# Kernel tuning notes

Hardware: AMD Instinct MI355X
Metric: run time of the kernel (lower is better)

Reference implementation:

```python
import jax, jax.numpy as jnp
import numpy as np

M_GROUPS = 512  # fixed number of segments (== fill_max for ii)


def setup_inputs() -> dict:
    key = jax.random.key(0)
    ks = jax.random.split(key, 8)
    B, N, D = 4, 16384, 384
    x = jax.random.normal(ks[0], (B, N, D), dtype=jnp.float32)
    ii = jax.random.randint(ks[1], (N,), 0, M_GROUPS)
    s = 1.0 / np.sqrt(D)
    f_w = jax.random.uniform(ks[2], (D, D), jnp.float32, -s, s)
    f_b = jax.random.uniform(ks[3], (D,), jnp.float32, -s, s)
    g_w = jax.random.uniform(ks[4], (D, D), jnp.float32, -s, s)
    g_b = jax.random.uniform(ks[5], (D,), jnp.float32, -s, s)
    h_w = jax.random.uniform(ks[6], (D, D), jnp.float32, -s, s)
    h_b = jax.random.uniform(ks[7], (D,), jnp.float32, -s, s)
    return {"x": x, "ii": ii, "f_w": f_w, "f_b": f_b,
            "g_w": g_w, "g_b": g_b, "h_w": h_w, "h_b": h_b}


def reference(x, ii, f_w, f_b, g_w, g_b, h_w, h_b):
    # x: [B, N, D], ii: [N] group indices in [0, M_GROUPS)
    logits = x @ g_w.T + g_b                      # g(x): [B, N, D]
    exp_logits = jnp.exp(logits)
    # segment sum over n for each group m (== one-hot einsum 'bnm,bnd->bmd')
    seg = lambda e: jax.ops.segment_sum(e, ii, num_segments=M_GROUPS)
    sum_exp = jax.vmap(seg)(exp_logits)           # [B, M, D]
    denom = sum_exp[:, ii]                        # gather back: [B, N, D]
    w = exp_logits / (denom + 1e-6)
    fx = x @ f_w.T + f_b                          # f(x): [B, N, D]
    y = jax.vmap(seg)(fx * w)                     # [B, M, D]
    y = y @ h_w.T + h_b                           # h(y)
    return y[:, ii]                               # expand: [B, N, D]
```

## Files before the change

kernel.cpp:

```cpp
#include <hip/hip_runtime.h>
#include <hip/hip_bf16.h>

#define D 384
#define NROWS 16384
#define BATCH 4
#define MG 512
#define RTOT (BATCH * NROWS)
#define NC (2 * D)
#define JB 64
#define NJB (D / JB)
#define BM 128
#define BK 32
#define NKT (D / BK)
#define NMT (RTOT / BM)

typedef __attribute__((ext_vector_type(8))) short bf16x8;
typedef __attribute__((ext_vector_type(4))) float f32x4;

static __device__ __forceinline__ unsigned short f2bf(float f) {
  unsigned int u = __float_as_uint(f);
  unsigned int r = u + 0x7fffu + ((u >> 16) & 1u);
  return (unsigned short)(r >> 16);
}
static __device__ __forceinline__ unsigned int cvtpk(float lo, float hi) {
  unsigned int r;
  asm("v_cvt_pk_bf16_f32 %0, %1, %2" : "=v"(r) : "v"(lo), "v"(hi));
  return r;
}
static __device__ __forceinline__ float frcp(float f) {
  float r;
  asm("v_rcp_f32 %0, %1" : "=v"(r) : "v"(f));
  return r;
}

typedef __attribute__((address_space(1))) const void gvoid_t;
typedef __attribute__((address_space(3))) void lvoid_t;
static __device__ __forceinline__ void gl16(const void* g, void* l) {
  __builtin_amdgcn_global_load_lds((gvoid_t*)g, (lvoid_t*)l, 16, 0, 0);
}

__global__ __launch_bounds__(256) void k_convert(const float* __restrict__ x,
                                                 unsigned short* __restrict__ xb) {
  const long total8 = (long)RTOT * D / 8;
  for (long i = blockIdx.x * (long)blockDim.x + threadIdx.x; i < total8;
       i += (long)gridDim.x * blockDim.x) {
    const float4 v0 = ((const float4*)x)[2 * i];
    const float4 v1 = ((const float4*)x)[2 * i + 1];
    int4 o;
    o.x = cvtpk(v0.x, v0.y);
    o.y = cvtpk(v0.z, v0.w);
    o.z = cvtpk(v1.x, v1.y);
    o.w = cvtpk(v1.z, v1.w);
    ((int4*)xb)[i] = o;
  }
}

__global__ __launch_bounds__(512) void k_prep(
    const int* __restrict__ ii, const float* __restrict__ g_w,
    const float* __restrict__ f_w, const float* __restrict__ h_w,
    unsigned short* __restrict__ wt2, unsigned short* __restrict__ hw,
    int* __restrict__ csr_rows, int* __restrict__ grp_sorted,
    float* __restrict__ s12) {
  __shared__ int cnt[MG];
  __shared__ int scan[MG];
  const int blk = blockIdx.x;
  const int t = threadIdx.x;
  if (blk == 0) {
    cnt[t] = 0;
    __syncthreads();
    for (int n = t; n < NROWS; n += MG) atomicAdd(&cnt[ii[n]], 1);
    __syncthreads();
    const int v = cnt[t];
    scan[t] = v;
    __syncthreads();
#pragma unroll
    for (int o = 1; o < MG; o <<= 1) {
      int u = (t >= o) ? scan[t - o] : 0;
      __syncthreads();
      scan[t] += u;
      __syncthreads();
    }
    cnt[t] = scan[t] - v;
    __syncthreads();
    for (int n = t; n < NROWS; n += MG) {
      int m = ii[n];
      int pos = atomicAdd(&cnt[m], 1);
      csr_rows[pos] = n;
      grp_sorted[pos] = m;
    }
  } else if (blk < 64) {
    const int tot4 = 2 * BATCH * MG * D / 4;
    float4 z = {0.f, 0.f, 0.f, 0.f};
    for (int i = (blk - 1) * 512 + t; i < tot4; i += 63 * 512) ((float4*)s12)[i] = z;
  } else {
    const int tid0 = (blk - 64) * 512 + t;
    const int stride = 64 * 512;
    for (int idx = tid0; idx < NC * D; idx += stride) {
      int jblk = idx / (128 * D);
      int rem = idx % (128 * D);
      int c = rem / D, k = rem % D;
      int j = jblk * JB + (c & 63);
      float v = (c < JB) ? g_w[j * D + k] : f_w[j * D + k];
      wt2[idx] = f2bf(v);
    }
    for (int idx = tid0; idx < D * D; idx += stride) hw[idx] = f2bf(h_w[idx]);
  }
}

__global__ __launch_bounds__(256, 4) void k_gemm1(
    const unsigned short* __restrict__ xb, const unsigned short* __restrict__ wt2,
    const float* __restrict__ g_b, const float* __restrict__ f_b,
    const int* __restrict__ csr_rows, const int* __restrict__ grp_sorted,
    float* __restrict__ s1acc, float* __restrict__ s2acc) {
  __shared__ __attribute__((aligned(16))) unsigned short As[2][BM * BK];
  __shared__ __attribute__((aligned(16))) unsigned short Bs[2][BM * BK];
  __shared__ int grpS[BM];

  const int wg = blockIdx.x;
  const int xcd = wg & 7;
  const int ix = wg >> 3;
  const int mt = xcd * (NMT / 8) + ix / NJB;
  const int jb = ix % NJB;
  const int b = mt >> 7;
  const int ib = (mt & 127) * BM;
  const int j0 = jb * JB;

  const int tid = threadIdx.x;
  const int lane = tid & 63, wid = tid >> 6;
  const int wr = wid >> 1, wc = wid & 1;

  if (tid < BM) grpS[tid] = grp_sorted[ib + tid];

  const int srow = wid * 32 + (lane >> 2);
  const int skb = (((lane & 3) ^ ((lane >> 3) & 3))) * 16;
  const int arow0 = b * NROWS + csr_rows[ib + srow];
  const int arow1 = b * NROWS + csr_rows[ib + srow + 16];
  const char* aS0 = (const char*)xb + (size_t)arow0 * (D * 2) + skb;
  const char* aS1 = (const char*)xb + (size_t)arow1 * (D * 2) + skb;
  const char* bS0 = (const char*)wt2 + (size_t)jb * (128 * D * 2) + (size_t)srow * (D * 2) + skb;
  const char* bS1 = bS0 + 16 * (D * 2);

  f32x4 acc[4][4];
#pragma unroll
  for (int m = 0; m < 4; m++)
#pragma unroll
    for (int n = 0; n < 4; n++) acc[m][n] = (f32x4){0.f, 0.f, 0.f, 0.f};

  {
    char* ad = (char*)As[0] + wid * 2048;
    char* bd = (char*)Bs[0] + wid * 2048;
    gl16(aS0, ad); gl16(aS1, ad + 1024);
    gl16(bS0, bd); gl16(bS1, bd + 1024);
  }
  __syncthreads();

  const int swz16 = (((lane >> 4) ^ ((lane >> 1) & 3))) * 16;

#pragma unroll 1
  for (int kt = 0; kt < NKT; ++kt) {
    const int cur = kt & 1;
    if (kt < NKT - 1) {
      const int kb = (kt + 1) * (BK * 2);
      char* ad = (char*)As[cur ^ 1] + wid * 2048;
      char* bd = (char*)Bs[cur ^ 1] + wid * 2048;
      gl16(aS0 + kb, ad); gl16(aS1 + kb, ad + 1024);
      gl16(bS0 + kb, bd); gl16(bS1 + kb, bd + 1024);
    }
    bf16x8 af[4], bfv[4];
#pragma unroll
    for (int m = 0; m < 4; m++)
      af[m] = *(const bf16x8*)((const char*)&As[cur][0] +
                               (wr * 64 + m * 16 + (lane & 15)) * 64 + swz16);
#pragma unroll
    for (int n = 0; n < 4; n++) {
      const int c = (n < 2) ? (wc * 32 + n * 16) : (64 + wc * 32 + (n - 2) * 16);
      bfv[n] = *(const bf16x8*)((const char*)&Bs[cur][0] + (c + (lane & 15)) * 64 + swz16);
    }
#pragma unroll
    for (int m = 0; m < 4; m++)
#pragma unroll
      for (int n = 0; n < 4; n++)
        acc[m][n] = __builtin_amdgcn_mfma_f32_16x16x32_bf16(af[m], bfv[n], acc[m][n], 0, 0, 0);
    __syncthreads();
  }

  const int jA = j0 + wc * 32 + (lane & 15);
  const float gb0 = g_b[jA], gb1 = g_b[jA + 16];
  const float fb0 = f_b[jA], fb1 = f_b[jA + 16];

  int gmr[4][4];
#pragma unroll
  for (int m = 0; m < 4; m++)
#pragma unroll
    for (int r = 0; r < 4; r++)
      gmr[m][r] = grpS[wr * 64 + m * 16 + (lane >> 4) * 4 + r];

#pragma unroll
  for (int m = 0; m < 4; m++)
#pragma unroll
    for (int r = 0; r < 4; r++) {
      const float e0 = expf(acc[m][0][r] + gb0);
      const float e1 = expf(acc[m][1][r] + gb1);
      const float f0 = acc[m][2][r] + fb0;
      const float f1 = acc[m][3][r] + fb1;
      acc[m][0][r] = e0; acc[m][1][r] = e1;
      acc[m][2][r] = f0 * e0; acc[m][3][r] = f1 * e1;
    }

  const int gLo = grpS[wr * 64], gHi = grpS[wr * 64 + 63];
  for (int g = gLo; g <= gHi; ++g) {
    float v0 = 0.f, v1 = 0.f, v2 = 0.f, v3 = 0.f;
#pragma unroll
    for (int m = 0; m < 4; m++)
#pragma unroll
      for (int r = 0; r < 4; r++)
        if (gmr[m][r] == g) {
          v0 += acc[m][0][r]; v1 += acc[m][1][r];
          v2 += acc[m][2][r]; v3 += acc[m][3][r];
        }
    v0 += __shfl_xor(v0, 16); v0 += __shfl_xor(v0, 32);
    v1 += __shfl_xor(v1, 16); v1 += __shfl_xor(v1, 32);
    v2 += __shfl_xor(v2, 16); v2 += __shfl_xor(v2, 32);
    v3 += __shfl_xor(v3, 16); v3 += __shfl_xor(v3, 32);
    if (lane < 16) {
      float* s1p = s1acc + ((size_t)(b * MG + g)) * D + j0 + wc * 32 + lane;
      float* s2p = s2acc + ((size_t)(b * MG + g)) * D + j0 + wc * 32 + lane;
      atomicAdd(s1p, v0);
      atomicAdd(s1p + 16, v1);
      atomicAdd(s2p, v2);
      atomicAdd(s2p + 16, v3);
    }
  }
}

__global__ __launch_bounds__(256) void k_gemm2(
    const float* __restrict__ s1, const float* __restrict__ s2,
    const unsigned short* __restrict__ hw, const float* __restrict__ h_b,
    float* __restrict__ outpre) {
  const int tid = threadIdx.x, lane = tid & 63, wid = tid >> 6;
  const int r0 = blockIdx.y * 16;
  const int c0 = blockIdx.x * 64 + wid * 16;
  f32x4 acc = (f32x4){0.f, 0.f, 0.f, 0.f};
  const int arow = r0 + (lane & 15);
  const float* s1p = s1 + (size_t)arow * D + (lane >> 4) * 8;
  const float* s2p = s2 + (size_t)arow * D + (lane >> 4) * 8;
  const unsigned short* bRow = hw + (size_t)(c0 + (lane & 15)) * D + (lane >> 4) * 8;
#pragma unroll
  for (int kt = 0; kt < D / 32; kt++) {
    float4 u0 = *(const float4*)(s1p + kt * 32);
    float4 u1 = *(const float4*)(s1p + kt * 32 + 4);
    float4 w0 = *(const float4*)(s2p + kt * 32);
    float4 w1 = *(const float4*)(s2p + kt * 32 + 4);
    int4 yi;
    yi.x = cvtpk(w0.x * frcp(u0.x + 1e-6f), w0.y * frcp(u0.y + 1e-6f));
    yi.y = cvtpk(w0.z * frcp(u0.z + 1e-6f), w0.w * frcp(u0.w + 1e-6f));
    yi.z = cvtpk(w1.x * frcp(u1.x + 1e-6f), w1.y * frcp(u1.y + 1e-6f));
    yi.w = cvtpk(w1.z * frcp(u1.z + 1e-6f), w1.w * frcp(u1.w + 1e-6f));
    bf16x8 af = *(bf16x8*)&yi;
    bf16x8 bf_ = *(const bf16x8*)(bRow + kt * 32);
    acc = __builtin_amdgcn_mfma_f32_16x16x32_bf16(af, bf_, acc, 0, 0, 0);
  }
  const int col = c0 + (lane & 15);
  const float hb = h_b[col];
#pragma unroll
  for (int r = 0; r < 4; r++) {
    const int row = r0 + (lane >> 4) * 4 + r;
    outpre[(size_t)row * D + col] = acc[r] + hb;
  }
}

__global__ void k_gather(const float* __restrict__ outpre, const int* __restrict__ ii,
                         float* __restrict__ out) {
  const long total4 = (long)RTOT * (D / 4);
  for (long i = blockIdx.x * (long)blockDim.x + threadIdx.x; i < total4;
       i += (long)gridDim.x * blockDim.x) {
    const long row = i / (D / 4);
    const int q = (int)(i % (D / 4));
    const int b = (int)(row >> 14);
    const int n = (int)(row & (NROWS - 1));
    const int g = ii[n];
    ((float4*)out)[i] = ((const float4*)outpre)[((size_t)(b * MG + g)) * (D / 4) + q];
  }
}

extern "C" void kernel_launch(void* const* d_in, const int* in_sizes, int n_in,
                              void* d_out, int out_size, void* d_ws, size_t ws_size,
                              hipStream_t stream) {
  const float* x = (const float*)d_in[0];
  const int* ii = (const int*)d_in[1];
  const float* f_w = (const float*)d_in[2];
  const float* f_b = (const float*)d_in[3];
  const float* g_w = (const float*)d_in[4];
  const float* g_b = (const float*)d_in[5];
  const float* h_w = (const float*)d_in[6];
  const float* h_b = (const float*)d_in[7];
  float* out = (float*)d_out;

  char* ws = (char*)d_ws;
  size_t off = 0;
  auto alloc = [&](size_t bytes) {
    size_t p = off;
    off = (off + bytes + 255) & ~(size_t)255;
    return p;
  };
  unsigned short* xb = (unsigned short*)(ws + alloc((size_t)RTOT * D * 2));
  unsigned short* wt2 = (unsigned short*)(ws + alloc((size_t)NC * D * 2));
  unsigned short* hw = (unsigned short*)(ws + alloc((size_t)D * D * 2));
  float* s1acc = (float*)(ws + alloc((size_t)BATCH * MG * D * 4));
  float* s2acc = (float*)(ws + alloc((size_t)BATCH * MG * D * 4));
  float* outpre = (float*)(ws + alloc((size_t)BATCH * MG * D * 4));
  int* csr_rows = (int*)(ws + alloc((size_t)NROWS * 4));
  int* grp_sorted = (int*)(ws + alloc((size_t)NROWS * 4));

  k_prep<<<dim3(128), dim3(512), 0, stream>>>(ii, g_w, f_w, h_w, wt2, hw, csr_rows,
                                              grp_sorted, s1acc);
  k_convert<<<dim3(4096), dim3(256), 0, stream>>>(x, xb);
  k_gemm1<<<dim3(NJB * NMT), dim3(256), 0, stream>>>(xb, wt2, g_b, f_b, csr_rows,
                                                     grp_sorted, s1acc, s2acc);
  k_gemm2<<<dim3(D / 64, (BATCH * MG) / 16), dim3(256), 0, stream>>>(s1acc, s2acc, hw, h_b,
                                                                     outpre);
  k_gather<<<dim3(4096), dim3(256), 0, stream>>>(outpre, ii, out);
}
```

Measured before the change: 155.6 us.

## Make gemm1 persistent with resident weight slice and pre-permuted sorted input rows

```diff
diff --git a/kernel.cpp b/kernel.cpp
--- a/kernel.cpp
+++ b/kernel.cpp
@@ -9,10 +9,7 @@
 #define NC (2 * D)
 #define JB 64
 #define NJB (D / JB)
-#define BM 128
-#define BK 32
-#define NKT (D / BK)
-#define NMT (RTOT / BM)
+#define NKT 12
 
 typedef __attribute__((ext_vector_type(8))) short bf16x8;
 typedef __attribute__((ext_vector_type(4))) float f32x4;
@@ -37,22 +34,6 @@
 typedef __attribute__((address_space(3))) void lvoid_t;
 static __device__ __forceinline__ void gl16(const void* g, void* l) {
   __builtin_amdgcn_global_load_lds((gvoid_t*)g, (lvoid_t*)l, 16, 0, 0);
-}
-
-__global__ __launch_bounds__(256) void k_convert(const float* __restrict__ x,
-                                                 unsigned short* __restrict__ xb) {
-  const long total8 = (long)RTOT * D / 8;
-  for (long i = blockIdx.x * (long)blockDim.x + threadIdx.x; i < total8;
-       i += (long)gridDim.x * blockDim.x) {
-    const float4 v0 = ((const float4*)x)[2 * i];
-    const float4 v1 = ((const float4*)x)[2 * i + 1];
-    int4 o;
-    o.x = cvtpk(v0.x, v0.y);
-    o.y = cvtpk(v0.z, v0.w);
-    o.z = cvtpk(v1.x, v1.y);
-    o.w = cvtpk(v1.z, v1.w);
-    ((int4*)xb)[i] = o;
-  }
 }
 
 __global__ __launch_bounds__(512) void k_prep(
@@ -107,38 +88,61 @@
   }
 }
 
-__global__ __launch_bounds__(256, 4) void k_gemm1(
-    const unsigned short* __restrict__ xb, const unsigned short* __restrict__ wt2,
+__global__ __launch_bounds__(256) void k_convert(const float* __restrict__ x,
+                                                 const int* __restrict__ csr_rows,
+                                                 unsigned short* __restrict__ xp) {
+  const int g = blockIdx.x * 256 + threadIdx.x;
+  const int orow = g / 48;
+  const int c = g - orow * 48;
+  const int bb = orow >> 14;
+  const int ir = csr_rows[orow & (NROWS - 1)];
+  const float* src = x + ((size_t)(bb << 14) + ir) * D + c * 8;
+  const float4 v0 = ((const float4*)src)[0];
+  const float4 v1 = ((const float4*)src)[1];
+  int4 o;
+  o.x = cvtpk(v0.x, v0.y);
+  o.y = cvtpk(v0.z, v0.w);
+  o.z = cvtpk(v1.x, v1.y);
+  o.w = cvtpk(v1.z, v1.w);
+  ((int4*)xp)[g] = o;
+}
+
+__global__ __launch_bounds__(512, 1) void k_gemm1(
+    const unsigned short* __restrict__ xp, const unsigned short* __restrict__ wt2,
     const float* __restrict__ g_b, const float* __restrict__ f_b,
-    const int* __restrict__ csr_rows, const int* __restrict__ grp_sorted,
-    float* __restrict__ s1acc, float* __restrict__ s2acc) {
-  __shared__ __attribute__((aligned(16))) unsigned short As[2][BM * BK];
-  __shared__ __attribute__((aligned(16))) unsigned short Bs[2][BM * BK];
-  __shared__ int grpS[BM];
-
-  const int wg = blockIdx.x;
-  const int xcd = wg & 7;
-  const int ix = wg >> 3;
-  const int mt = xcd * (NMT / 8) + ix / NJB;
-  const int jb = ix % NJB;
-  const int b = mt >> 7;
-  const int ib = (mt & 127) * BM;
-  const int j0 = jb * JB;
+    const int* __restrict__ grp_sorted, float* __restrict__ s1acc,
+    float* __restrict__ s2acc) {
+  __shared__ __attribute__((aligned(16))) unsigned short Bs[12 * 4096];
+  __shared__ __attribute__((aligned(16))) unsigned short As[4 * 8192];
 
   const int tid = threadIdx.x;
   const int lane = tid & 63, wid = tid >> 6;
-  const int wr = wid >> 1, wc = wid & 1;
-
-  if (tid < BM) grpS[tid] = grp_sorted[ib + tid];
-
-  const int srow = wid * 32 + (lane >> 2);
-  const int skb = (((lane & 3) ^ ((lane >> 3) & 3))) * 16;
-  const int arow0 = b * NROWS + csr_rows[ib + srow];
-  const int arow1 = b * NROWS + csr_rows[ib + srow + 16];
-  const char* aS0 = (const char*)xb + (size_t)arow0 * (D * 2) + skb;
-  const char* aS1 = (const char*)xb + (size_t)arow1 * (D * 2) + skb;
-  const char* bS0 = (const char*)wt2 + (size_t)jb * (128 * D * 2) + (size_t)srow * (D * 2) + skb;
-  const char* bS1 = bS0 + 16 * (D * 2);
+  const int h = wid >> 2;
+  const int w4 = wid & 3;
+  const int wr = w4 >> 1, wc = w4 & 1;
+  const int q0 = blockIdx.x * 6;
+  const int pair0 = q0 & 255;
+
+  const int skb = ((lane & 3) ^ ((lane >> 3) & 3)) * 16;
+  const int swz16 = ((lane >> 4) ^ ((lane >> 1) & 3)) * 16;
+
+  const char* p0 = (const char*)xp +
+                   ((size_t)(pair0 * 256 + h * 128 + w4 * 32 + (lane >> 2))) * (D * 2) + skb;
+  const char* p1 = p0 + 16 * (D * 2);
+  int ipair = pair0;
+
+  char* const AsB = (char*)As;
+  char* const BsB = (char*)Bs;
+  const int adoff = h * 8192 + w4 * 2048;
+
+#pragma unroll
+  for (int s = 0; s < 3; ++s) {
+    char* ad = AsB + s * 16384 + adoff;
+    gl16(p0, ad);
+    gl16(p1, ad + 1024);
+    p0 += 64;
+    p1 += 64;
+  }
 
   f32x4 acc[4][4];
 #pragma unroll
@@ -146,90 +150,115 @@
 #pragma unroll
     for (int n = 0; n < 4; n++) acc[m][n] = (f32x4){0.f, 0.f, 0.f, 0.f};
 
-  {
-    char* ad = (char*)As[0] + wid * 2048;
-    char* bd = (char*)Bs[0] + wid * 2048;
-    gl16(aS0, ad); gl16(aS1, ad + 1024);
-    gl16(bS0, bd); gl16(bS1, bd + 1024);
-  }
-  __syncthreads();
-
-  const int swz16 = (((lane >> 4) ^ ((lane >> 1) & 3))) * 16;
-
+  int jbprev = -1;
 #pragma unroll 1
-  for (int kt = 0; kt < NKT; ++kt) {
-    const int cur = kt & 1;
-    if (kt < NKT - 1) {
-      const int kb = (kt + 1) * (BK * 2);
-      char* ad = (char*)As[cur ^ 1] + wid * 2048;
-      char* bd = (char*)Bs[cur ^ 1] + wid * 2048;
-      gl16(aS0 + kb, ad); gl16(aS1 + kb, ad + 1024);
-      gl16(bS0 + kb, bd); gl16(bS1 + kb, bd + 1024);
-    }
-    bf16x8 af[4], bfv[4];
+  for (int e = 0; e < 6; ++e) {
+    const int q = q0 + e;
+    const int jb = q >> 8;
+    const int pair = q & 255;
+    const bool jch = (jb != jbprev);
+    jbprev = jb;
+    const char* wtj = (const char*)wt2 + (size_t)jb * (128 * D * 2);
+
+#pragma unroll
+    for (int kt = 0; kt < NKT; ++kt) {
+      asm volatile("s_waitcnt vmcnt(4)\ns_barrier" ::: "memory");
+      if (kt == 0 && jch) {
+#pragma unroll
+        for (int i = 0; i < 12; ++i)
+          gl16(wtj + (size_t)(tid >> 2) * (D * 2) + i * 64 + skb,
+               BsB + i * 8192 + wid * 1024);
+        asm volatile("s_waitcnt vmcnt(0)\ns_barrier" ::: "memory");
+      }
+      {
+        char* ad = AsB + ((kt + 3) & 3) * 16384 + adoff;
+        gl16(p0, ad);
+        gl16(p1, ad + 1024);
+        if (kt == 8) {
+          p0 += 195904; p1 += 195904;
+          if (++ipair == 256) {
+            ipair = 0;
+            p0 -= (size_t)256 * 196608;
+            p1 -= (size_t)256 * 196608;
+          }
+        } else {
+          p0 += 64; p1 += 64;
+        }
+      }
+      bf16x8 af[4], bfv[4];
+      const char* ab = AsB + (kt & 3) * 16384 + h * 8192;
+#pragma unroll
+      for (int m = 0; m < 4; m++)
+        af[m] = *(const bf16x8*)(ab + (wr * 64 + m * 16 + (lane & 15)) * 64 + swz16);
+      const char* bbp = BsB + kt * 8192;
+#pragma unroll
+      for (int n = 0; n < 4; n++) {
+        const int c = (n < 2) ? (wc * 32 + n * 16) : (64 + wc * 32 + (n - 2) * 16);
+        bfv[n] = *(const bf16x8*)(bbp + (c + (lane & 15)) * 64 + swz16);
+      }
+#pragma unroll
+      for (int m = 0; m < 4; m++)
+#pragma unroll
+        for (int n = 0; n < 4; n++)
+          acc[m][n] = __builtin_amdgcn_mfma_f32_16x16x32_bf16(af[m], bfv[n], acc[m][n], 0, 0, 0);
+    }
+
+    {
+      const int j0 = jb * JB;
+      const int jA = j0 + wc * 32 + (lane & 15);
+      const float gb0 = g_b[jA], gb1 = g_b[jA + 16];
+      const float fb0 = f_b[jA], fb1 = f_b[jA + 16];
+      const int rowbase = (pair & 63) * 256 + h * 128 + wr * 64;
+      const int bb2 = pair >> 6;
+
+      int gmr[4][4];
+#pragma unroll
+      for (int m = 0; m < 4; m++)
+#pragma unroll
+        for (int r = 0; r < 4; r++)
+          gmr[m][r] = grp_sorted[rowbase + m * 16 + (lane >> 4) * 4 + r];
+
+#pragma unroll
+      for (int m = 0; m < 4; m++)
+#pragma unroll
+        for (int r = 0; r < 4; r++) {
+          const float e0 = expf(acc[m][0][r] + gb0);
+          const float e1 = expf(acc[m][1][r] + gb1);
+          const float f0 = acc[m][2][r] + fb0;
+          const float f1 = acc[m][3][r] + fb1;
+          acc[m][0][r] = e0; acc[m][1][r] = e1;
+          acc[m][2][r] = f0 * e0; acc[m][3][r] = f1 * e1;
+        }
+
+      const int gLo = grp_sorted[rowbase], gHi = grp_sorted[rowbase + 63];
+      for (int g = gLo; g <= gHi; ++g) {
+        float v0 = 0.f, v1 = 0.f, v2 = 0.f, v3 = 0.f;
+#pragma unroll
+        for (int m = 0; m < 4; m++)
+#pragma unroll
+          for (int r = 0; r < 4; r++)
+            if (gmr[m][r] == g) {
+              v0 += acc[m][0][r]; v1 += acc[m][1][r];
+              v2 += acc[m][2][r]; v3 += acc[m][3][r];
+            }
+        v0 += __shfl_xor(v0, 16); v0 += __shfl_xor(v0, 32);
+        v1 += __shfl_xor(v1, 16); v1 += __shfl_xor(v1, 32);
+        v2 += __shfl_xor(v2, 16); v2 += __shfl_xor(v2, 32);
+        v3 += __shfl_xor(v3, 16); v3 += __shfl_xor(v3, 32);
+        if (lane < 16) {
+          float* s1p = s1acc + ((size_t)(bb2 * MG + g)) * D + j0 + wc * 32 + lane;
+          float* s2p = s2acc + ((size_t)(bb2 * MG + g)) * D + j0 + wc * 32 + lane;
+          atomicAdd(s1p, v0);
+          atomicAdd(s1p + 16, v1);
+          atomicAdd(s2p, v2);
+          atomicAdd(s2p + 16, v3);
+        }
+      }
+    }
 #pragma unroll
     for (int m = 0; m < 4; m++)
-      af[m] = *(const bf16x8*)((const char*)&As[cur][0] +
-                               (wr * 64 + m * 16 + (lane & 15)) * 64 + swz16);
-#pragma unroll
-    for (int n = 0; n < 4; n++) {
-      const int c = (n < 2) ? (wc * 32 + n * 16) : (64 + wc * 32 + (n - 2) * 16);
-      bfv[n] = *(const bf16x8*)((const char*)&Bs[cur][0] + (c + (lane & 15)) * 64 + swz16);
-    }
-#pragma unroll
-    for (int m = 0; m < 4; m++)
-#pragma unroll
-      for (int n = 0; n < 4; n++)
-        acc[m][n] = __builtin_amdgcn_mfma_f32_16x16x32_bf16(af[m], bfv[n], acc[m][n], 0, 0, 0);
-    __syncthreads();
-  }
-
-  const int jA = j0 + wc * 32 + (lane & 15);
-  const float gb0 = g_b[jA], gb1 = g_b[jA + 16];
-  const float fb0 = f_b[jA], fb1 = f_b[jA + 16];
-
-  int gmr[4][4];
-#pragma unroll
-  for (int m = 0; m < 4; m++)
-#pragma unroll
-    for (int r = 0; r < 4; r++)
-      gmr[m][r] = grpS[wr * 64 + m * 16 + (lane >> 4) * 4 + r];
-
-#pragma unroll
-  for (int m = 0; m < 4; m++)
-#pragma unroll
-    for (int r = 0; r < 4; r++) {
-      const float e0 = expf(acc[m][0][r] + gb0);
-      const float e1 = expf(acc[m][1][r] + gb1);
-      const float f0 = acc[m][2][r] + fb0;
-      const float f1 = acc[m][3][r] + fb1;
-      acc[m][0][r] = e0; acc[m][1][r] = e1;
-      acc[m][2][r] = f0 * e0; acc[m][3][r] = f1 * e1;
-    }
-
-  const int gLo = grpS[wr * 64], gHi = grpS[wr * 64 + 63];
-  for (int g = gLo; g <= gHi; ++g) {
-    float v0 = 0.f, v1 = 0.f, v2 = 0.f, v3 = 0.f;
-#pragma unroll
-    for (int m = 0; m < 4; m++)
-#pragma unroll
-      for (int r = 0; r < 4; r++)
-        if (gmr[m][r] == g) {
-          v0 += acc[m][0][r]; v1 += acc[m][1][r];
-          v2 += acc[m][2][r]; v3 += acc[m][3][r];
-        }
-    v0 += __shfl_xor(v0, 16); v0 += __shfl_xor(v0, 32);
-    v1 += __shfl_xor(v1, 16); v1 += __shfl_xor(v1, 32);
-    v2 += __shfl_xor(v2, 16); v2 += __shfl_xor(v2, 32);
-    v3 += __shfl_xor(v3, 16); v3 += __shfl_xor(v3, 32);
-    if (lane < 16) {
-      float* s1p = s1acc + ((size_t)(b * MG + g)) * D + j0 + wc * 32 + lane;
-      float* s2p = s2acc + ((size_t)(b * MG + g)) * D + j0 + wc * 32 + lane;
-      atomicAdd(s1p, v0);
-      atomicAdd(s1p + 16, v1);
-      atomicAdd(s2p, v2);
-      atomicAdd(s2p + 16, v3);
-    }
+#pragma unroll
+      for (int n = 0; n < 4; n++) acc[m][n] = (f32x4){0.f, 0.f, 0.f, 0.f};
   }
 }
 
@@ -303,7 +332,7 @@
     off = (off + bytes + 255) & ~(size_t)255;
     return p;
   };
-  unsigned short* xb = (unsigned short*)(ws + alloc((size_t)RTOT * D * 2));
+  unsigned short* xp = (unsigned short*)(ws + alloc((size_t)RTOT * D * 2));
   unsigned short* wt2 = (unsigned short*)(ws + alloc((size_t)NC * D * 2));
   unsigned short* hw = (unsigned short*)(ws + alloc((size_t)D * D * 2));
   float* s1acc = (float*)(ws + alloc((size_t)BATCH * MG * D * 4));
@@ -314,9 +343,8 @@
 
   k_prep<<<dim3(128), dim3(512), 0, stream>>>(ii, g_w, f_w, h_w, wt2, hw, csr_rows,
                                               grp_sorted, s1acc);
-  k_convert<<<dim3(4096), dim3(256), 0, stream>>>(x, xb);
-  k_gemm1<<<dim3(NJB * NMT), dim3(256), 0, stream>>>(xb, wt2, g_b, f_b, csr_rows,
-                                                     grp_sorted, s1acc, s2acc);
+  k_convert<<<dim3(RTOT * (D / 8) / 256), dim3(256), 0, stream>>>(x, csr_rows, xp);
+  k_gemm1<<<dim3(256), dim3(512), 0, stream>>>(xp, wt2, g_b, f_b, grp_sorted, s1acc, s2acc);
   k_gemm2<<<dim3(D / 64, (BATCH * MG) / 16), dim3(256), 0, stream>>>(s1acc, s2acc, hw, h_b,
                                                                      outpre);
   k_gather<<<dim3(4096), dim3(256), 0, stream>>>(outpre, ii, out);
```

Measured after the change: 158.2 us. Within noise of the previous version (+1.7%).

## Fuse x conversion into GEMM1 with LDS-resident A tile across all columns

Applied to the files above, without the earlier changes.

```diff
diff --git a/kernel.cpp b/kernel.cpp
--- a/kernel.cpp
+++ b/kernel.cpp
@@ -9,10 +9,7 @@
 #define NC (2 * D)
 #define JB 64
 #define NJB (D / JB)
-#define BM 128
-#define BK 32
-#define NKT (D / BK)
-#define NMT (RTOT / BM)
+#define NKT 12
 
 typedef __attribute__((ext_vector_type(8))) short bf16x8;
 typedef __attribute__((ext_vector_type(4))) float f32x4;
@@ -37,22 +34,6 @@
 typedef __attribute__((address_space(3))) void lvoid_t;
 static __device__ __forceinline__ void gl16(const void* g, void* l) {
   __builtin_amdgcn_global_load_lds((gvoid_t*)g, (lvoid_t*)l, 16, 0, 0);
-}
-
-__global__ __launch_bounds__(256) void k_convert(const float* __restrict__ x,
-                                                 unsigned short* __restrict__ xb) {
-  const long total8 = (long)RTOT * D / 8;
-  for (long i = blockIdx.x * (long)blockDim.x + threadIdx.x; i < total8;
-       i += (long)gridDim.x * blockDim.x) {
-    const float4 v0 = ((const float4*)x)[2 * i];
-    const float4 v1 = ((const float4*)x)[2 * i + 1];
-    int4 o;
-    o.x = cvtpk(v0.x, v0.y);
-    o.y = cvtpk(v0.z, v0.w);
-    o.z = cvtpk(v1.x, v1.y);
-    o.w = cvtpk(v1.z, v1.w);
-    ((int4*)xb)[i] = o;
-  }
 }
 
 __global__ __launch_bounds__(512) void k_prep(
@@ -107,38 +88,56 @@
   }
 }
 
-__global__ __launch_bounds__(256, 4) void k_gemm1(
-    const unsigned short* __restrict__ xb, const unsigned short* __restrict__ wt2,
+__global__ __launch_bounds__(512, 1) void k_gemm1(
+    const float* __restrict__ x, const unsigned short* __restrict__ wt2,
     const float* __restrict__ g_b, const float* __restrict__ f_b,
     const int* __restrict__ csr_rows, const int* __restrict__ grp_sorted,
     float* __restrict__ s1acc, float* __restrict__ s2acc) {
-  __shared__ __attribute__((aligned(16))) unsigned short As[2][BM * BK];
-  __shared__ __attribute__((aligned(16))) unsigned short Bs[2][BM * BK];
-  __shared__ int grpS[BM];
-
-  const int wg = blockIdx.x;
-  const int xcd = wg & 7;
-  const int ix = wg >> 3;
-  const int mt = xcd * (NMT / 8) + ix / NJB;
-  const int jb = ix % NJB;
-  const int b = mt >> 7;
-  const int ib = (mt & 127) * BM;
-  const int j0 = jb * JB;
+  __shared__ __attribute__((aligned(16))) unsigned short As[NKT * 4096];
+  __shared__ __attribute__((aligned(16))) unsigned short Bs[2][2][4096];
+  __shared__ int grpS[128];
 
   const int tid = threadIdx.x;
   const int lane = tid & 63, wid = tid >> 6;
-  const int wr = wid >> 1, wc = wid & 1;
-
-  if (tid < BM) grpS[tid] = grp_sorted[ib + tid];
-
-  const int srow = wid * 32 + (lane >> 2);
-  const int skb = (((lane & 3) ^ ((lane >> 3) & 3))) * 16;
-  const int arow0 = b * NROWS + csr_rows[ib + srow];
-  const int arow1 = b * NROWS + csr_rows[ib + srow + 16];
-  const char* aS0 = (const char*)xb + (size_t)arow0 * (D * 2) + skb;
-  const char* aS1 = (const char*)xb + (size_t)arow1 * (D * 2) + skb;
-  const char* bS0 = (const char*)wt2 + (size_t)jb * (128 * D * 2) + (size_t)srow * (D * 2) + skb;
-  const char* bS1 = bS0 + 16 * (D * 2);
+  const int wr = wid >> 2;
+  const int wq = wid & 3;
+  const int p = wq >> 1;
+  const int u = wq & 1;
+  const int blk = blockIdx.x;
+  const int b = blk >> 7;
+  const int ibl = (blk & 127) * 128;
+
+  if (tid < 128) grpS[tid] = grp_sorted[ibl + tid];
+
+  const int skb = ((lane & 3) ^ ((lane >> 3) & 3)) * 16;
+  const int swz16 = ((lane >> 4) ^ ((lane >> 1) & 3)) * 16;
+
+  const char* wtb = (const char*)wt2;
+  const int prow = wid * 16 + (lane >> 2);
+  const size_t bsrcoff = (size_t)prow * (D * 2) + skb;
+  char* const bdstw = (char*)&Bs[0][0][0];
+  gl16(wtb + 0 * (128 * D * 2) + bsrcoff, bdstw + wid * 1024);
+  gl16(wtb + 1 * (128 * D * 2) + bsrcoff, bdstw + 8192 + wid * 1024);
+
+  {
+    const int arow = tid >> 2;
+    const int grow = csr_rows[ibl + arow];
+    const float* asrc = x + ((size_t)((b << 14) + grow)) * D + (tid & 3) * 8;
+    const int aslot = (tid & 3) ^ ((tid >> 3) & 3);
+    char* adst = (char*)As + arow * 64 + aslot * 16;
+#pragma unroll
+    for (int kt = 0; kt < NKT; ++kt) {
+      const float4 v0 = *(const float4*)(asrc + kt * 32);
+      const float4 v1 = *(const float4*)(asrc + kt * 32 + 4);
+      int4 o;
+      o.x = cvtpk(v0.x, v0.y);
+      o.y = cvtpk(v0.z, v0.w);
+      o.z = cvtpk(v1.x, v1.y);
+      o.w = cvtpk(v1.z, v1.w);
+      *(int4*)(adst + kt * 8192) = o;
+    }
+  }
+  __syncthreads();
 
   f32x4 acc[4][4];
 #pragma unroll
@@ -146,90 +145,93 @@
 #pragma unroll
     for (int n = 0; n < 4; n++) acc[m][n] = (f32x4){0.f, 0.f, 0.f, 0.f};
 
-  {
-    char* ad = (char*)As[0] + wid * 2048;
-    char* bd = (char*)Bs[0] + wid * 2048;
-    gl16(aS0, ad); gl16(aS1, ad + 1024);
-    gl16(bS0, bd); gl16(bS1, bd + 1024);
-  }
-  __syncthreads();
-
-  const int swz16 = (((lane >> 4) ^ ((lane >> 1) & 3))) * 16;
-
 #pragma unroll 1
-  for (int kt = 0; kt < NKT; ++kt) {
-    const int cur = kt & 1;
-    if (kt < NKT - 1) {
-      const int kb = (kt + 1) * (BK * 2);
-      char* ad = (char*)As[cur ^ 1] + wid * 2048;
-      char* bd = (char*)Bs[cur ^ 1] + wid * 2048;
-      gl16(aS0 + kb, ad); gl16(aS1 + kb, ad + 1024);
-      gl16(bS0 + kb, bd); gl16(bS1 + kb, bd + 1024);
-    }
-    bf16x8 af[4], bfv[4];
+  for (int e = 0; e < 3; ++e) {
+#pragma unroll
+    for (int kt = 0; kt < NKT; ++kt) {
+      asm volatile("s_waitcnt vmcnt(0)\ns_barrier" ::: "memory");
+      if (!(e == 2 && kt == 11)) {
+        const int kt2 = (kt == 11) ? 0 : kt + 1;
+        const int jbn = (kt == 11) ? 2 * e + 2 : 2 * e;
+        char* nd = (char*)&Bs[(kt + 1) & 1][0][0] + wid * 1024;
+        gl16(wtb + (size_t)jbn * (128 * D * 2) + kt2 * 64 + bsrcoff, nd);
+        gl16(wtb + (size_t)(jbn + 1) * (128 * D * 2) + kt2 * 64 + bsrcoff, nd + 8192);
+      }
+      bf16x8 af[4], bfv[4];
+      const char* ab = (const char*)As + kt * 8192;
+#pragma unroll
+      for (int m = 0; m < 4; m++)
+        af[m] = *(const bf16x8*)(ab + (wr * 64 + m * 16 + (lane & 15)) * 64 + swz16);
+      const char* bb = (const char*)&Bs[kt & 1][p][0];
+#pragma unroll
+      for (int n = 0; n < 4; n++) {
+        const int c = (n < 2) ? (u * 32 + n * 16) : (64 + u * 32 + (n - 2) * 16);
+        bfv[n] = *(const bf16x8*)(bb + (c + (lane & 15)) * 64 + swz16);
+      }
+      __builtin_amdgcn_s_setprio(1);
+#pragma unroll
+      for (int m = 0; m < 4; m++)
+#pragma unroll
+        for (int n = 0; n < 4; n++)
+          acc[m][n] = __builtin_amdgcn_mfma_f32_16x16x32_bf16(af[m], bfv[n], acc[m][n], 0, 0, 0);
+      __builtin_amdgcn_s_setprio(0);
+    }
+
+    {
+      const int j0 = (2 * e + p) * JB;
+      const int jA = j0 + u * 32 + (lane & 15);
+      const float gb0 = g_b[jA], gb1 = g_b[jA + 16];
+      const float fb0 = f_b[jA], fb1 = f_b[jA + 16];
+      const int rowbase = wr * 64;
+
+      int gmr[4][4];
+#pragma unroll
+      for (int m = 0; m < 4; m++)
+#pragma unroll
+        for (int r = 0; r < 4; r++)
+          gmr[m][r] = grpS[rowbase + m * 16 + (lane >> 4) * 4 + r];
+
+#pragma unroll
+      for (int m = 0; m < 4; m++)
+#pragma unroll
+        for (int r = 0; r < 4; r++) {
+          const float e0 = expf(acc[m][0][r] + gb0);
+          const float e1 = expf(acc[m][1][r] + gb1);
+          const float f0 = acc[m][2][r] + fb0;
+          const float f1 = acc[m][3][r] + fb1;
+          acc[m][0][r] = e0; acc[m][1][r] = e1;
+          acc[m][2][r] = f0 * e0; acc[m][3][r] = f1 * e1;
+        }
+
+      const int gLo = grpS[rowbase], gHi = grpS[rowbase + 63];
+      for (int g = gLo; g <= gHi; ++g) {
+        float v0 = 0.f, v1 = 0.f, v2 = 0.f, v3 = 0.f;
+#pragma unroll
+        for (int m = 0; m < 4; m++)
+#pragma unroll
+          for (int r = 0; r < 4; r++)
+            if (gmr[m][r] == g) {
+              v0 += acc[m][0][r]; v1 += acc[m][1][r];
+              v2 += acc[m][2][r]; v3 += acc[m][3][r];
+            }
+        v0 += __shfl_xor(v0, 16); v0 += __shfl_xor(v0, 32);
+        v1 += __shfl_xor(v1, 16); v1 += __shfl_xor(v1, 32);
+        v2 += __shfl_xor(v2, 16); v2 += __shfl_xor(v2, 32);
+        v3 += __shfl_xor(v3, 16); v3 += __shfl_xor(v3, 32);
+        if (lane < 16) {
+          float* s1p = s1acc + ((size_t)(b * MG + g)) * D + j0 + u * 32 + lane;
+          float* s2p = s2acc + ((size_t)(b * MG + g)) * D + j0 + u * 32 + lane;
+          atomicAdd(s1p, v0);
+          atomicAdd(s1p + 16, v1);
+          atomicAdd(s2p, v2);
+          atomicAdd(s2p + 16, v3);
+        }
+      }
+    }
 #pragma unroll
     for (int m = 0; m < 4; m++)
-      af[m] = *(const bf16x8*)((const char*)&As[cur][0] +
-                               (wr * 64 + m * 16 + (lane & 15)) * 64 + swz16);
-#pragma unroll
-    for (int n = 0; n < 4; n++) {
-      const int c = (n < 2) ? (wc * 32 + n * 16) : (64 + wc * 32 + (n - 2) * 16);
-      bfv[n] = *(const bf16x8*)((const char*)&Bs[cur][0] + (c + (lane & 15)) * 64 + swz16);
-    }
-#pragma unroll
-    for (int m = 0; m < 4; m++)
-#pragma unroll
-      for (int n = 0; n < 4; n++)
-        acc[m][n] = __builtin_amdgcn_mfma_f32_16x16x32_bf16(af[m], bfv[n], acc[m][n], 0, 0, 0);
-    __syncthreads();
-  }
-
-  const int jA = j0 + wc * 32 + (lane & 15);
-  const float gb0 = g_b[jA], gb1 = g_b[jA + 16];
-  const float fb0 = f_b[jA], fb1 = f_b[jA + 16];
-
-  int gmr[4][4];
-#pragma unroll
-  for (int m = 0; m < 4; m++)
-#pragma unroll
-    for (int r = 0; r < 4; r++)
-      gmr[m][r] = grpS[wr * 64 + m * 16 + (lane >> 4) * 4 + r];
-
-#pragma unroll
-  for (int m = 0; m < 4; m++)
-#pragma unroll
-    for (int r = 0; r < 4; r++) {
-      const float e0 = expf(acc[m][0][r] + gb0);
-      const float e1 = expf(acc[m][1][r] + gb1);
-      const float f0 = acc[m][2][r] + fb0;
-      const float f1 = acc[m][3][r] + fb1;
-      acc[m][0][r] = e0; acc[m][1][r] = e1;
-      acc[m][2][r] = f0 * e0; acc[m][3][r] = f1 * e1;
-    }
-
-  const int gLo = grpS[wr * 64], gHi = grpS[wr * 64 + 63];
-  for (int g = gLo; g <= gHi; ++g) {
-    float v0 = 0.f, v1 = 0.f, v2 = 0.f, v3 = 0.f;
-#pragma unroll
-    for (int m = 0; m < 4; m++)
-#pragma unroll
-      for (int r = 0; r < 4; r++)
-        if (gmr[m][r] == g) {
-          v0 += acc[m][0][r]; v1 += acc[m][1][r];
-          v2 += acc[m][2][r]; v3 += acc[m][3][r];
-        }
-    v0 += __shfl_xor(v0, 16); v0 += __shfl_xor(v0, 32);
-    v1 += __shfl_xor(v1, 16); v1 += __shfl_xor(v1, 32);
-    v2 += __shfl_xor(v2, 16); v2 += __shfl_xor(v2, 32);
-    v3 += __shfl_xor(v3, 16); v3 += __shfl_xor(v3, 32);
-    if (lane < 16) {
-      float* s1p = s1acc + ((size_t)(b * MG + g)) * D + j0 + wc * 32 + lane;
-      float* s2p = s2acc + ((size_t)(b * MG + g)) * D + j0 + wc * 32 + lane;
-      atomicAdd(s1p, v0);
-      atomicAdd(s1p + 16, v1);
-      atomicAdd(s2p, v2);
-      atomicAdd(s2p + 16, v3);
-    }
+#pragma unroll
+      for (int n = 0; n < 4; n++) acc[m][n] = (f32x4){0.f, 0.f, 0.f, 0.f};
   }
 }
 
@@ -303,7 +305,6 @@
     off = (off + bytes + 255) & ~(size_t)255;
     return p;
   };
-  unsigned short* xb = (unsigned short*)(ws + alloc((size_t)RTOT * D * 2));
   unsigned short* wt2 = (unsigned short*)(ws + alloc((size_t)NC * D * 2));
   unsigned short* hw = (unsigned short*)(ws + alloc((size_t)D * D * 2));
   float* s1acc = (float*)(ws + alloc((size_t)BATCH * MG * D * 4));
@@ -314,9 +315,8 @@
 
   k_prep<<<dim3(128), dim3(512), 0, stream>>>(ii, g_w, f_w, h_w, wt2, hw, csr_rows,
                                               grp_sorted, s1acc);
-  k_convert<<<dim3(4096), dim3(256), 0, stream>>>(x, xb);
-  k_gemm1<<<dim3(NJB * NMT), dim3(256), 0, stream>>>(xb, wt2, g_b, f_b, csr_rows,
-                                                     grp_sorted, s1acc, s2acc);
+  k_gemm1<<<dim3(512), dim3(512), 0, stream>>>(x, wt2, g_b, f_b, csr_rows, grp_sorted,
+                                               s1acc, s2acc);
   k_gemm2<<<dim3(D / 64, (BATCH * MG) / 16), dim3(256), 0, stream>>>(s1acc, s2acc, hw, h_b,
                                                                      outpre);
   k_gather<<<dim3(4096), dim3(256), 0, stream>>>(outpre, ii, out);
```

Result: faster. 150.3 us (-3.4%).
